# Kernel optimization log

Hardware: AMD Instinct MI355X
Metric: run time of the kernel (lower is better)

## Reference

```python
import jax, jax.numpy as jnp
import numpy as np

GAMMA = 0.5
BATCH, DIM, UNITS = 16384, 512, 1024


def setup_inputs() -> dict:
    key = jax.random.key(0)
    k1, k2 = jax.random.split(key)
    inputs = jax.random.normal(k1, (BATCH, DIM), dtype=jnp.float32)
    mu = jax.random.normal(k2, (DIM, UNITS), dtype=jnp.float32)
    return {"inputs": inputs, "mu": mu}


def reference(inputs, mu):
    # Squared L2 distance from each input row to each center (column of mu):
    x_sq = jnp.sum(inputs * inputs, axis=1, keepdims=True)        # [B, 1]
    mu_sq = jnp.sum(mu * mu, axis=0, keepdims=True)               # [1, U]
    cross = inputs @ mu                                           # [B, U] GEMM
    l2 = x_sq - 2.0 * cross + mu_sq                                # [B, U]
    return jnp.exp(-GAMMA * l2)
```

## Files before the change

### kernel.cpp

```cpp
#include <hip/hip_runtime.h>
#include <hip/hip_bf16.h>

#define BATCH 16384
#define DIM   512
#define UNITS 1024

typedef float v16f __attribute__((ext_vector_type(16)));

__device__ __forceinline__ void async_copy16(const void* g, void* l) {
    __builtin_amdgcn_global_load_lds(
        (const __attribute__((address_space(1))) void*)g,
        (__attribute__((address_space(3))) void*)l,
        16 , 0 , 0 );
}

__global__ __launch_bounds__(256)
void prep_kernel(const float* __restrict__ in, const float* __restrict__ mu,
                 unsigned char* __restrict__ A8, unsigned char* __restrict__ B8,
                 float* __restrict__ xsq, float* __restrict__ musq) {
    __shared__ float lds[64][65];
    __shared__ float red[64][4];
    const int t = threadIdx.x;
    if (blockIdx.x < BATCH / 4) {
        const int lane = t & 63;
        const int row  = blockIdx.x * 4 + (t >> 6);
        const float4* src = (const float4*)(in + (size_t)row * DIM);
        float4 a = src[lane * 2];
        float4 b = src[lane * 2 + 1];
        float s = a.x * a.x + a.y * a.y + a.z * a.z + a.w * a.w
                + b.x * b.x + b.y * b.y + b.z * b.z + b.w * b.w;
        int lo = __builtin_amdgcn_cvt_pk_fp8_f32(a.x, a.y, 0, false);
        lo     = __builtin_amdgcn_cvt_pk_fp8_f32(a.z, a.w, lo, true);
        int hi = __builtin_amdgcn_cvt_pk_fp8_f32(b.x, b.y, 0, false);
        hi     = __builtin_amdgcn_cvt_pk_fp8_f32(b.z, b.w, hi, true);
        *(int2*)(A8 + (size_t)row * DIM + lane * 8) = make_int2(lo, hi);
        for (int off = 32; off; off >>= 1) s += __shfl_down(s, off, 64);
        if (lane == 0) xsq[row] = s;
    } else {
        const int n0 = (blockIdx.x - BATCH / 4) * 64;
        const int c  = t & 63, r4 = t >> 6;
        const int nl = t >> 2, kp = t & 3;
        float s = 0.f;
        for (int kc = 0; kc < DIM; kc += 64) {
            __syncthreads();
#pragma unroll
            for (int i = 0; i < 16; i++)
                lds[r4 + i * 4][c] = mu[(size_t)(kc + r4 + i * 4) * UNITS + n0 + c];
            __syncthreads();
            int wr[4];
#pragma unroll
            for (int q = 0; q < 4; q++) {
                float f0 = lds[kp * 16 + q * 4 + 0][nl];
                float f1 = lds[kp * 16 + q * 4 + 1][nl];
                float f2 = lds[kp * 16 + q * 4 + 2][nl];
                float f3 = lds[kp * 16 + q * 4 + 3][nl];
                s += f0 * f0 + f1 * f1 + f2 * f2 + f3 * f3;
                int v = __builtin_amdgcn_cvt_pk_fp8_f32(f0, f1, 0, false);
                wr[q]  = __builtin_amdgcn_cvt_pk_fp8_f32(f2, f3, v, true);
            }
            *(int4*)(B8 + (size_t)(n0 + nl) * DIM + kc + kp * 16) =
                make_int4(wr[0], wr[1], wr[2], wr[3]);
        }
        red[nl][kp] = s;
        __syncthreads();
        if (t < 64) musq[n0 + t] = red[t][0] + red[t][1] + red[t][2] + red[t][3];
    }
}

__global__ __launch_bounds__(256, 4)
void rbf_gemm_kernel(const unsigned char* __restrict__ A8,
                     const unsigned char* __restrict__ B8,
                     const float* __restrict__ xsq,
                     const float* __restrict__ musq,
                     float* __restrict__ out) {
    __shared__ __attribute__((aligned(16))) unsigned char As[128 * 128];
    __shared__ __attribute__((aligned(16))) unsigned char Bs[128 * 128];

    const int t   = threadIdx.x;
    const int l   = t & 63;
    const int wv  = t >> 6;
    const int ln  = l & 31;
    const int h   = l >> 5;
    const int wmr = (wv >> 1) * 64;
    const int wnr = (wv & 1) * 64;

    const int g   = blockIdx.x;
    const int mt  = (g & 7) * 16 + (g >> 6);
    const int nt  = (g >> 3) & 7;
    const int m0  = mt * 128;
    const int n0  = nt * 128;

    v16f acc[2][2];
#pragma unroll
    for (int i = 0; i < 2; i++)
#pragma unroll
        for (int j = 0; j < 2; j++) acc[i][j] = (v16f)0.f;

    const int srow = t >> 3;
    const int gsl  = (t & 7) ^ (srow & 7);
    const unsigned char* ga = A8 + (size_t)(m0 + srow) * DIM + gsl * 16;
    const unsigned char* gb = B8 + (size_t)(n0 + srow) * DIM + gsl * 16;
    const int sw = ln & 7;

    for (int kt = 0; kt < 4; kt++) {
        const int kc = kt * 128;
        if (kt) __syncthreads();
#pragma unroll
        for (int i = 0; i < 4; i++) {
            async_copy16(ga + (size_t)i * 32 * DIM + kc, As + i * 4096 + t * 16);
            async_copy16(gb + (size_t)i * 32 * DIM + kc, Bs + i * 4096 + t * 16);
        }
        __syncthreads();

#pragma unroll
        for (int w = 0; w < 8; w++) {
            const int so = ((w ^ sw) * 16) + 8 * h;
            long a0 = *(const long*)(As + (wmr + ln) * 128 + so);
            long a1 = *(const long*)(As + (wmr + 32 + ln) * 128 + so);
            long b0 = *(const long*)(Bs + (wnr + ln) * 128 + so);
            long b1 = *(const long*)(Bs + (wnr + 32 + ln) * 128 + so);
            acc[0][0] = __builtin_amdgcn_mfma_f32_32x32x16_fp8_fp8(a0, b0, acc[0][0], 0, 0, 0);
            acc[0][1] = __builtin_amdgcn_mfma_f32_32x32x16_fp8_fp8(a0, b1, acc[0][1], 0, 0, 0);
            acc[1][0] = __builtin_amdgcn_mfma_f32_32x32x16_fp8_fp8(a1, b0, acc[1][0], 0, 0, 0);
            acc[1][1] = __builtin_amdgcn_mfma_f32_32x32x16_fp8_fp8(a1, b1, acc[1][1], 0, 0, 0);
        }
    }

    const float xv = -0.5f * xsq[m0 + wmr + l];
#pragma unroll
    for (int ti = 0; ti < 2; ti++) {
#pragma unroll
        for (int tj = 0; tj < 2; tj++) {
            const int c0 = n0 + wnr + tj * 32 + ln;
            const float mb = -0.5f * musq[c0];
#pragma unroll
            for (int r = 0; r < 16; r++) {
                const int rl = (r & 3) + 8 * (r >> 2) + 4 * h;
                const float xb = __shfl(xv, ti * 32 + rl, 64);
                float v = __expf(acc[ti][tj][r] + xb + mb);
                __builtin_nontemporal_store(
                    v, out + (size_t)(m0 + wmr + ti * 32 + rl) * UNITS + c0);
            }
        }
    }
}

extern "C" void kernel_launch(void* const* d_in, const int* in_sizes, int n_in,
                              void* d_out, int out_size, void* d_ws, size_t ws_size,
                              hipStream_t stream) {
    const float* inputs = (const float*)d_in[0];
    const float* mu     = (const float*)d_in[1];
    float* out = (float*)d_out;

    char* ws = (char*)d_ws;
    unsigned char* A8 = (unsigned char*)ws;
    unsigned char* B8 = (unsigned char*)(ws + (size_t)BATCH * DIM);
    float* xsq  = (float*)(ws + (size_t)BATCH * DIM + (size_t)UNITS * DIM);
    float* musq = xsq + BATCH;

    prep_kernel<<<BATCH / 4 + UNITS / 64, 256, 0, stream>>>(
        inputs, mu, A8, B8, xsq, musq);
    rbf_gemm_kernel<<<(BATCH / 128) * (UNITS / 128), 256, 0, stream>>>(
        A8, B8, xsq, musq, out);
}
```

Before: 125.3 us.

## Keep B fragments in registers and stream A directly from global without LDS

The GEMM kernel drops the LDS staging and async global-to-LDS copies. Each wave now holds a full 32-column slice of B (all of K) in registers. It streams 32-row A fragments straight from global memory through four chunks per block, with no barriers. The grid is remapped to 1024 blocks covering 128 rows by 128 columns each. This removes LDS traffic and synchronisation. In exchange, A is loaded from global in uncoalesced 8-byte pieces and reused less, and the large register footprint may cut occupancy.

```diff
diff --git a/kernel.cpp b/kernel.cpp
--- a/kernel.cpp
+++ b/kernel.cpp
@@ -6,13 +6,6 @@
 #define UNITS 1024
 
 typedef float v16f __attribute__((ext_vector_type(16)));
-
-__device__ __forceinline__ void async_copy16(const void* g, void* l) {
-    __builtin_amdgcn_global_load_lds(
-        (const __attribute__((address_space(1))) void*)g,
-        (__attribute__((address_space(3))) void*)l,
-        16 , 0 , 0 );
-}
 
 __global__ __launch_bounds__(256)
 void prep_kernel(const float* __restrict__ in, const float* __restrict__ mu,
@@ -73,74 +66,46 @@
                      const float* __restrict__ xsq,
                      const float* __restrict__ musq,
                      float* __restrict__ out) {
-    __shared__ __attribute__((aligned(16))) unsigned char As[128 * 128];
-    __shared__ __attribute__((aligned(16))) unsigned char Bs[128 * 128];
+    const int t  = threadIdx.x;
+    const int l  = t & 63;
+    const int w  = t >> 6;
+    const int ln = l & 31;
+    const int h  = l >> 5;
 
-    const int t   = threadIdx.x;
-    const int l   = t & 63;
-    const int wv  = t >> 6;
-    const int ln  = l & 31;
-    const int h   = l >> 5;
-    const int wmr = (wv >> 1) * 64;
-    const int wnr = (wv & 1) * 64;
+    const int b   = blockIdx.x;
+    const int x   = b & 7;
+    const int q   = b >> 3;
+    const int rg  = q & 15;
+    const int cgq = q >> 4;
+    const int m0  = x * 2048 + rg * 128;
+    const int n0  = (cgq * 4 + w) * 32;
 
-    const int g   = blockIdx.x;
-    const int mt  = (g & 7) * 16 + (g >> 6);
-    const int nt  = (g >> 3) & 7;
-    const int m0  = mt * 128;
-    const int n0  = nt * 128;
+    const unsigned char* bp = B8 + (size_t)(n0 + ln) * DIM + h * 8;
+    long bfrag[32];
+#pragma unroll
+    for (int kw = 0; kw < 32; kw++)
+        bfrag[kw] = *(const long*)(bp + kw * 16);
 
-    v16f acc[2][2];
+    const float mb = -0.5f * musq[n0 + ln];
+
+#pragma unroll 1
+    for (int c = 0; c < 4; c++) {
+        const int mc = m0 + c * 32;
+        const unsigned char* ap = A8 + (size_t)(mc + ln) * DIM + h * 8;
+        v16f acc = (v16f)0.f;
 #pragma unroll
-    for (int i = 0; i < 2; i++)
+        for (int kw = 0; kw < 32; kw++) {
+            long a = *(const long*)(ap + kw * 16);
+            acc = __builtin_amdgcn_mfma_f32_32x32x16_fp8_fp8(
+                a, bfrag[kw], acc, 0, 0, 0);
+        }
 #pragma unroll
-        for (int j = 0; j < 2; j++) acc[i][j] = (v16f)0.f;
-
-    const int srow = t >> 3;
-    const int gsl  = (t & 7) ^ (srow & 7);
-    const unsigned char* ga = A8 + (size_t)(m0 + srow) * DIM + gsl * 16;
-    const unsigned char* gb = B8 + (size_t)(n0 + srow) * DIM + gsl * 16;
-    const int sw = ln & 7;
-
-    for (int kt = 0; kt < 4; kt++) {
-        const int kc = kt * 128;
-        if (kt) __syncthreads();
-#pragma unroll
-        for (int i = 0; i < 4; i++) {
-            async_copy16(ga + (size_t)i * 32 * DIM + kc, As + i * 4096 + t * 16);
-            async_copy16(gb + (size_t)i * 32 * DIM + kc, Bs + i * 4096 + t * 16);
-        }
-        __syncthreads();
-
-#pragma unroll
-        for (int w = 0; w < 8; w++) {
-            const int so = ((w ^ sw) * 16) + 8 * h;
-            long a0 = *(const long*)(As + (wmr + ln) * 128 + so);
-            long a1 = *(const long*)(As + (wmr + 32 + ln) * 128 + so);
-            long b0 = *(const long*)(Bs + (wnr + ln) * 128 + so);
-            long b1 = *(const long*)(Bs + (wnr + 32 + ln) * 128 + so);
-            acc[0][0] = __builtin_amdgcn_mfma_f32_32x32x16_fp8_fp8(a0, b0, acc[0][0], 0, 0, 0);
-            acc[0][1] = __builtin_amdgcn_mfma_f32_32x32x16_fp8_fp8(a0, b1, acc[0][1], 0, 0, 0);
-            acc[1][0] = __builtin_amdgcn_mfma_f32_32x32x16_fp8_fp8(a1, b0, acc[1][0], 0, 0, 0);
-            acc[1][1] = __builtin_amdgcn_mfma_f32_32x32x16_fp8_fp8(a1, b1, acc[1][1], 0, 0, 0);
-        }
-    }
-
-    const float xv = -0.5f * xsq[m0 + wmr + l];
-#pragma unroll
-    for (int ti = 0; ti < 2; ti++) {
-#pragma unroll
-        for (int tj = 0; tj < 2; tj++) {
-            const int c0 = n0 + wnr + tj * 32 + ln;
-            const float mb = -0.5f * musq[c0];
-#pragma unroll
-            for (int r = 0; r < 16; r++) {
-                const int rl = (r & 3) + 8 * (r >> 2) + 4 * h;
-                const float xb = __shfl(xv, ti * 32 + rl, 64);
-                float v = __expf(acc[ti][tj][r] + xb + mb);
-                __builtin_nontemporal_store(
-                    v, out + (size_t)(m0 + wmr + ti * 32 + rl) * UNITS + c0);
-            }
+        for (int r = 0; r < 16; r++) {
+            const int rl = (r & 3) + 8 * (r >> 2) + 4 * h;
+            const float xb = -0.5f * xsq[mc + rl];
+            float v = __expf(acc[r] + xb + mb);
+            __builtin_nontemporal_store(
+                v, out + (size_t)(mc + rl) * UNITS + n0 + ln);
         }
     }
 }
@@ -160,6 +125,5 @@
 
     prep_kernel<<<BATCH / 4 + UNITS / 64, 256, 0, stream>>>(
         inputs, mu, A8, B8, xsq, musq);
-    rbf_gemm_kernel<<<(BATCH / 128) * (UNITS / 128), 256, 0, stream>>>(
-        A8, B8, xsq, musq, out);
+    rbf_gemm_kernel<<<1024, 256, 0, stream>>>(A8, B8, xsq, musq, out);
 }
```

After: 167.5 us. 33.7% more time.
